# Kernel tuning notes

Measured on AMD Instinct MI355X. Metric: run time of the kernel, lower is better.

Reference implementation:

```python
import jax, jax.numpy as jnp
import numpy as np

B, C, H, W = 4, 128, 64, 64
HEADS, DH, MEM = 4, 32, 16
HID = HEADS * DH  # 128


def setup_inputs() -> dict:
    key = jax.random.key(0)
    k1, k2, k3, k4, k5 = jax.random.split(key, 5)
    return {
        "x": jax.random.normal(k1, (B, C, H, W), jnp.float32),
        "memory": jax.random.normal(k2, (1, C, 1, MEM), jnp.float32),
        "w_qkv": jax.random.normal(k3, (3 * HID, C), jnp.float32) * 0.05,  # conv1x1, bias=False
        "w_out": jax.random.normal(k4, (C, HID), jnp.float32) * 0.05,      # conv1x1 weight
        "b_out": jax.random.normal(k5, (C,), jnp.float32) * 0.01,          # conv1x1 bias
    }


def reference(x, memory, w_qkv, w_out, b_out):
    b, c, h, w = x.shape
    hw = h * w
    scale = DH ** -0.5

    # flatten spatial, append memory tokens along token axis
    x_flat = x.reshape(b, c, hw)                         # (b, c, hw)
    mem = jnp.broadcast_to(memory[:, :, 0, :], (b, c, MEM))
    x_ext = jnp.concatenate([x_flat, mem], axis=2)       # (b, c, n) n = hw + MEM

    # 1x1 conv QKV projection == channel matmul
    qkv = jnp.einsum('oc,bcn->bon', w_qkv, x_ext)        # (b, 3*HID, n)
    q, k, v = jnp.split(qkv, 3, axis=1)                  # each (b, HID, n)

    def to_heads(t):
        return t.reshape(b, HEADS, DH, -1)               # (b, h, d, n)

    q = to_heads(q) * scale
    k = to_heads(k)
    v = to_heads(v)

    sim = jnp.einsum('bhdi,bhdj->bhij', q, k)            # (b, h, n, n)
    attn = jax.nn.softmax(sim, axis=-1)                  # stable softmax (amax-sub inside)
    out = jnp.einsum('bhij,bhdj->bhid', attn, v)         # (b, h, n, d)

    out = out[:, :, :hw]                                 # drop memory-token queries
    out = out.transpose(0, 1, 3, 2).reshape(b, HID, h, w)  # b (h d) x y

    return jnp.einsum('oc,bchw->bohw', w_out, out) + b_out[None, :, None, None]
```

## Files before the change

### kernel.cpp

```cpp
#include <hip/hip_runtime.h>
#include <hip/hip_bf16.h>

constexpr int NQ   = 4096;
constexpr int NKV  = 4112;
constexpr int NP   = 4160;
constexpr int CDIM = 128;
constexpr float QSC = 0.17677669529663687f * 1.4426950408889634f;

typedef __attribute__((ext_vector_type(8)))  short bf16x8;
typedef __attribute__((ext_vector_type(4)))  short bf16x4;
typedef __attribute__((ext_vector_type(4)))  float f32x4;
typedef __attribute__((ext_vector_type(16))) float f32x16;

static __device__ __forceinline__ unsigned short bfbits(float f) {
  __hip_bfloat16 h = __float2bfloat16(f);
  return *reinterpret_cast<unsigned short*>(&h);
}
static __device__ __forceinline__ unsigned pk2(float a, float b) {
  return (unsigned)bfbits(a) | ((unsigned)bfbits(b) << 16);
}

__global__ __launch_bounds__(256) void k1_qkv(
    const float* __restrict__ x, const float* __restrict__ memry,
    const float* __restrict__ wqkv, const float* __restrict__ wout,
    __hip_bfloat16* __restrict__ Qt, __hip_bfloat16* __restrict__ Kt,
    __hip_bfloat16* __restrict__ Vt, __hip_bfloat16* __restrict__ Wb) {
  __shared__ __align__(16) __hip_bfloat16 xt[64][136];
  const int b  = blockIdx.y;
  const int nb = blockIdx.x * 64;
  const int t  = threadIdx.x;
  const int wv = t >> 6, ln = t & 63;

  if (blockIdx.x == 0 && b == 0) {
    for (int i = t; i < CDIM * CDIM; i += 256) Wb[i] = __float2bfloat16(wout[i]);
  }

  {
    const int n = nb + ln;
    #pragma unroll
    for (int i = 0; i < 16; ++i) {
      const int c = wv * 32 + 2 * i;
      float v0 = 0.f, v1 = 0.f;
      if (n < NQ)        { v0 = x[((size_t)b * CDIM + c) * NQ + n];
                           v1 = x[((size_t)b * CDIM + c + 1) * NQ + n]; }
      else if (n < NKV)  { v0 = memry[c * 16 + (n - NQ)];
                           v1 = memry[(c + 1) * 16 + (n - NQ)]; }
      *reinterpret_cast<unsigned*>(&xt[ln][c]) =
          (unsigned)bfbits(v0) | ((unsigned)bfbits(v1) << 16);
    }
  }
  __syncthreads();

  const int li = ln & 15, g = ln >> 4;
  bf16x8 xa[4][4];
  #pragma unroll
  for (int nt = 0; nt < 4; ++nt)
    #pragma unroll
    for (int k = 0; k < 4; ++k)
      xa[nt][k] = *reinterpret_cast<const bf16x8*>(&xt[nt * 16 + li][k * 32 + 8 * g]);

  #pragma unroll
  for (int oi = 0; oi < 6; ++oi) {
    const int ot = wv * 6 + oi;
    bf16x8 wf[4];
    #pragma unroll
    for (int k = 0; k < 4; ++k) {
      const float* wp = &wqkv[(size_t)(ot * 16 + li) * CDIM + k * 32 + 8 * g];
      const float4 f0 = *reinterpret_cast<const float4*>(wp);
      const float4 f1 = *reinterpret_cast<const float4*>(wp + 4);
      bf16x8 wc;
      wc[0] = (short)bfbits(f0.x); wc[1] = (short)bfbits(f0.y);
      wc[2] = (short)bfbits(f0.z); wc[3] = (short)bfbits(f0.w);
      wc[4] = (short)bfbits(f1.x); wc[5] = (short)bfbits(f1.y);
      wc[6] = (short)bfbits(f1.z); wc[7] = (short)bfbits(f1.w);
      wf[k] = wc;
    }
    #pragma unroll
    for (int nt = 0; nt < 4; ++nt) {
      f32x4 a; a[0] = a[1] = a[2] = a[3] = 0.f;
      if (ot < 16) {
        #pragma unroll
        for (int k = 0; k < 4; ++k)
          a = __builtin_amdgcn_mfma_f32_16x16x32_bf16(xa[nt][k], wf[k], a, 0, 0, 0);
        const int o = ot * 16 + li;
        const int h = (o >> 5) & 3, d = o & 31;
        if (ot < 8) {
          #pragma unroll
          for (int r = 0; r < 4; ++r) {
            const int n = nb + nt * 16 + 4 * g + r;
            Qt[((size_t)(b * 4 + h) * NP + n) * 32 + d] = __float2bfloat16(a[r] * QSC);
          }
        } else {
          #pragma unroll
          for (int r = 0; r < 4; ++r) {
            const int n = nb + nt * 16 + 4 * g + r;
            Kt[((size_t)(b * 4 + h) * NP + n) * 32 + d] = __float2bfloat16(a[r]);
          }
        }
      } else {
        #pragma unroll
        for (int k = 0; k < 4; ++k)
          a = __builtin_amdgcn_mfma_f32_16x16x32_bf16(wf[k], xa[nt][k], a, 0, 0, 0);
        #pragma unroll
        for (int r = 0; r < 4; ++r) {
          const int o = ot * 16 + 4 * g + r;
          const int h = (o >> 5) & 3, d = o & 31;
          const int n = nb + nt * 16 + li;
          Vt[((size_t)(b * 4 + h) * 32 + d) * NP + n] = __float2bfloat16(a[r]);
        }
      }
    }
  }
}


#if __has_builtin(__builtin_amdgcn_mfma_f32_32x32x8bf16_1k)
#define HAS_PV8 1
#else
#define HAS_PV8 0
#endif

__global__ __launch_bounds__(256, 2) void k2_attn(
    const __hip_bfloat16* __restrict__ Qt, const __hip_bfloat16* __restrict__ Kt,
    const __hip_bfloat16* __restrict__ Vt, __hip_bfloat16* __restrict__ att) {
  __shared__ __align__(16) unsigned char smem[16896];
  __hip_bfloat16* kbuf = (__hip_bfloat16*)smem;
  __hip_bfloat16* vbuf = (__hip_bfloat16*)(smem + 4096);
  float (*olds)[32][33] = (float(*)[32][33])smem;

  const int wg  = blockIdx.x;
  const int xcd = wg & 7;
  const int i   = wg >> 3;
  const int bh  = 2 * xcd + (i & 1);
  const int wv  = threadIdx.x >> 6, lane = threadIdx.x & 63;
  const int lq  = lane & 31, hi = lane >> 5;
  const int qb  = (i >> 1) * 128 + wv * 32;

  const bf16x8 qf0 = *reinterpret_cast<const bf16x8*>(
      Qt + ((size_t)bh * NP + qb + lq) * 32 + 8 * hi);
  const bf16x8 qf1 = *reinterpret_cast<const bf16x8*>(
      Qt + ((size_t)bh * NP + qb + lq) * 32 + 16 + 8 * hi);

  const __hip_bfloat16* Ksrc = Kt + ((size_t)bh * NP + (wv >> 1) * 32 + lq) * 32
                                  + (wv & 1) * 16 + 8 * hi;
  const __hip_bfloat16* Vsrc = Vt + ((size_t)bh * 32 + lq) * NP + wv * 16 + 8 * hi;
  __hip_bfloat16* kdst = kbuf + wv * 512 + lane * 8;
  __hip_bfloat16* vdst = vbuf + wv * 512 + lane * 8;

  f32x16 acc0, acc1, z;
  #pragma unroll
  for (int q = 0; q < 16; ++q) { acc0[q] = 0.f; acc1[q] = 0.f; z[q] = 0.f; }
  float l0 = 0.f, l1 = 0.f, l2 = 0.f, l3 = 0.f;

  bf16x8 kreg = *reinterpret_cast<const bf16x8*>(Ksrc);
  bf16x8 vreg = *reinterpret_cast<const bf16x8*>(Vsrc);

  for (int t = 0; t < 64; ++t) {
    *reinterpret_cast<bf16x8*>(kdst) = kreg;
    *reinterpret_cast<bf16x8*>(vdst) = vreg;
    __syncthreads();
    if (t < 63) {
      kreg = *reinterpret_cast<const bf16x8*>(Ksrc + (size_t)(t + 1) * 2048);
      vreg = *reinterpret_cast<const bf16x8*>(Vsrc + (t + 1) * 64);
    }
    #pragma unroll
    for (int st = 0; st < 2; ++st) {
      const bf16x8 kf0 = *reinterpret_cast<const bf16x8*>(kbuf + st * 1024 + lane * 8);
      const bf16x8 kf1 = *reinterpret_cast<const bf16x8*>(kbuf + st * 1024 + 512 + lane * 8);
      f32x16 s = __builtin_amdgcn_mfma_f32_32x32x16_bf16(kf0, qf0, z, 0, 0, 0);
      s = __builtin_amdgcn_mfma_f32_32x32x16_bf16(kf1, qf1, s, 0, 0, 0);
      float p[16];
      #pragma unroll
      for (int r = 0; r < 16; ++r) p[r] = __builtin_amdgcn_exp2f(s[r]);
      l0 += (p[0] + p[1]) + (p[2] + p[3]);
      l1 += (p[4] + p[5]) + (p[6] + p[7]);
      l2 += (p[8] + p[9]) + (p[10] + p[11]);
      l3 += (p[12] + p[13]) + (p[14] + p[15]);
#if HAS_PV8
      union UU { unsigned u[2]; bf16x4 v; };
      UU a0, a1, a2, a3;
      a0.u[0] = pk2(p[0], p[1]);   a0.u[1] = pk2(p[2], p[3]);
      a1.u[0] = pk2(p[4], p[5]);   a1.u[1] = pk2(p[6], p[7]);
      a2.u[0] = pk2(p[8], p[9]);   a2.u[1] = pk2(p[10], p[11]);
      a3.u[0] = pk2(p[12], p[13]); a3.u[1] = pk2(p[14], p[15]);
      const __hip_bfloat16* vb = vbuf + st * 1024 + lq * 8 + hi * 4;
      const bf16x4 vf0 = *reinterpret_cast<const bf16x4*>(vb);
      const bf16x4 vf1 = *reinterpret_cast<const bf16x4*>(vb + 256);
      const bf16x4 vf2 = *reinterpret_cast<const bf16x4*>(vb + 512);
      const bf16x4 vf3 = *reinterpret_cast<const bf16x4*>(vb + 768);
      acc0 = __builtin_amdgcn_mfma_f32_32x32x8bf16_1k(a0.v, vf0, acc0, 0, 0, 0);
      acc0 = __builtin_amdgcn_mfma_f32_32x32x8bf16_1k(a1.v, vf1, acc0, 0, 0, 0);
      acc1 = __builtin_amdgcn_mfma_f32_32x32x8bf16_1k(a2.v, vf2, acc1, 0, 0, 0);
      acc1 = __builtin_amdgcn_mfma_f32_32x32x8bf16_1k(a3.v, vf3, acc1, 0, 0, 0);
#else
      unsigned a0u0 = pk2(p[0], p[1]),   a0u1 = pk2(p[2], p[3]);
      unsigned a1u0 = pk2(p[4], p[5]),   a1u1 = pk2(p[6], p[7]);
      unsigned a2u0 = pk2(p[8], p[9]),   a2u1 = pk2(p[10], p[11]);
      unsigned a3u0 = pk2(p[12], p[13]), a3u1 = pk2(p[14], p[15]);
      union U8 { unsigned u[4]; bf16x8 v; };
      const bf16x8 vh0 = *reinterpret_cast<const bf16x8*>(vbuf + (2 * st) * 512 + lane * 8);
      const bf16x8 vh1 = *reinterpret_cast<const bf16x8*>(vbuf + (2 * st + 1) * 512 + lane * 8);
      {
        const unsigned s0 = __shfl_xor(hi ? a0u0 : a1u0, 32, 64);
        const unsigned s1 = __shfl_xor(hi ? a0u1 : a1u1, 32, 64);
        U8 f;
        f.u[0] = hi ? s0 : a0u0; f.u[1] = hi ? s1 : a0u1;
        f.u[2] = hi ? a1u0 : s0; f.u[3] = hi ? a1u1 : s1;
        acc0 = __builtin_amdgcn_mfma_f32_32x32x16_bf16(f.v, vh0, acc0, 0, 0, 0);
      }
      {
        const unsigned s0 = __shfl_xor(hi ? a2u0 : a3u0, 32, 64);
        const unsigned s1 = __shfl_xor(hi ? a2u1 : a3u1, 32, 64);
        U8 f;
        f.u[0] = hi ? s0 : a2u0; f.u[1] = hi ? s1 : a2u1;
        f.u[2] = hi ? a3u0 : s0; f.u[3] = hi ? a3u1 : s1;
        acc1 = __builtin_amdgcn_mfma_f32_32x32x16_bf16(f.v, vh1, acc1, 0, 0, 0);
      }
#endif
    }
    __syncthreads();
  }

  {
    const __hip_bfloat16* Kp   = Kt + (size_t)bh * NP * 32 + (size_t)lq * 32 + 8 * hi;
    const __hip_bfloat16* Vrow = Vt + ((size_t)bh * 32 + lq) * NP;
    const int kb = 4096;
    const bf16x8 kf0 = *reinterpret_cast<const bf16x8*>(Kp + (size_t)kb * 32);
    const bf16x8 kf1 = *reinterpret_cast<const bf16x8*>(Kp + (size_t)kb * 32 + 16);
    f32x16 s = __builtin_amdgcn_mfma_f32_32x32x16_bf16(kf0, qf0, z, 0, 0, 0);
    s = __builtin_amdgcn_mfma_f32_32x32x16_bf16(kf1, qf1, s, 0, 0, 0);
    float p[8];
    #pragma unroll
    for (int r = 0; r < 8; ++r) p[r] = __builtin_amdgcn_exp2f(s[r]);
    l0 += (p[0] + p[1]) + (p[2] + p[3]);
    l1 += (p[4] + p[5]) + (p[6] + p[7]);
#if HAS_PV8
    union UU { unsigned u[2]; bf16x4 v; };
    UU a0, a1;
    a0.u[0] = pk2(p[0], p[1]); a0.u[1] = pk2(p[2], p[3]);
    a1.u[0] = pk2(p[4], p[5]); a1.u[1] = pk2(p[6], p[7]);
    const bf16x4 vf0 = *reinterpret_cast<const bf16x4*>(Vrow + kb + 4 * hi);
    const bf16x4 vf1 = *reinterpret_cast<const bf16x4*>(Vrow + kb + 8 + 4 * hi);
    acc0 = __builtin_amdgcn_mfma_f32_32x32x8bf16_1k(a0.v, vf0, acc0, 0, 0, 0);
    acc0 = __builtin_amdgcn_mfma_f32_32x32x8bf16_1k(a1.v, vf1, acc0, 0, 0, 0);
#else
    unsigned a0u0 = pk2(p[0], p[1]), a0u1 = pk2(p[2], p[3]);
    unsigned a1u0 = pk2(p[4], p[5]), a1u1 = pk2(p[6], p[7]);
    union U8 { unsigned u[4]; bf16x8 v; };
    const unsigned s0 = __shfl_xor(hi ? a0u0 : a1u0, 32, 64);
    const unsigned s1 = __shfl_xor(hi ? a0u1 : a1u1, 32, 64);
    U8 f;
    f.u[0] = hi ? s0 : a0u0; f.u[1] = hi ? s1 : a0u1;
    f.u[2] = hi ? a1u0 : s0; f.u[3] = hi ? a1u1 : s1;
    const bf16x8 vf = *reinterpret_cast<const bf16x8*>(Vrow + kb + 8 * hi);
    acc0 = __builtin_amdgcn_mfma_f32_32x32x16_bf16(f.v, vf, acc0, 0, 0, 0);
#endif
  }

  float lsum = (l0 + l1) + (l2 + l3);
  lsum += __shfl_xor(lsum, 32, 64);
  const float inv = 1.f / lsum;

  __syncthreads();
  #pragma unroll
  for (int r = 0; r < 16; ++r)
    olds[wv][(r & 3) + 8 * (r >> 2) + 4 * hi][lq] = acc0[r] + acc1[r];
  __syncthreads();

  __hip_bfloat16* dst = att + ((size_t)bh * NQ + qb + lq) * 32 + hi * 16;
  unsigned wbuf[8];
  #pragma unroll
  for (int j = 0; j < 8; ++j)
    wbuf[j] = pk2(olds[wv][lq][hi * 16 + 2 * j] * inv,
                  olds[wv][lq][hi * 16 + 2 * j + 1] * inv);
  *reinterpret_cast<uint4*>(dst)     = make_uint4(wbuf[0], wbuf[1], wbuf[2], wbuf[3]);
  *reinterpret_cast<uint4*>(dst + 8) = make_uint4(wbuf[4], wbuf[5], wbuf[6], wbuf[7]);
}

__global__ __launch_bounds__(256) void k3_proj(
    const __hip_bfloat16* __restrict__ att, const __hip_bfloat16* __restrict__ Wb,
    const float* __restrict__ bout, float* __restrict__ out) {
  const int b = blockIdx.y, nb = blockIdx.x * 64;
  const int wv = threadIdx.x >> 6, lane = threadIdx.x & 63;
  const int li = lane & 15, g = lane >> 4;

  bf16x8 wf[2][4];
  float bo[2][4];
  #pragma unroll
  for (int tt = 0; tt < 2; ++tt) {
    const int ot = 2 * wv + tt;
    #pragma unroll
    for (int k = 0; k < 4; ++k)
      wf[tt][k] = *reinterpret_cast<const bf16x8*>(
          &Wb[(size_t)(ot * 16 + li) * CDIM + k * 32 + 8 * g]);
    #pragma unroll
    for (int r = 0; r < 4; ++r) bo[tt][r] = bout[ot * 16 + 4 * g + r];
  }
  #pragma unroll
  for (int nt = 0; nt < 4; ++nt) {
    bf16x8 bfr[4];
    #pragma unroll
    for (int k = 0; k < 4; ++k)
      bfr[k] = *reinterpret_cast<const bf16x8*>(
          &att[(((size_t)(b * 4 + k)) * NQ + nb + nt * 16 + li) * 32 + 8 * g]);
    #pragma unroll
    for (int tt = 0; tt < 2; ++tt) {
      f32x4 a; a[0] = a[1] = a[2] = a[3] = 0.f;
      #pragma unroll
      for (int k = 0; k < 4; ++k)
        a = __builtin_amdgcn_mfma_f32_16x16x32_bf16(wf[tt][k], bfr[k], a, 0, 0, 0);
      const int ot = 2 * wv + tt;
      #pragma unroll
      for (int r = 0; r < 4; ++r)
        out[((size_t)b * CDIM + ot * 16 + 4 * g + r) * NQ + nb + nt * 16 + li] =
            a[r] + bo[tt][r];
    }
  }
}

extern "C" void kernel_launch(void* const* d_in, const int* in_sizes, int n_in,
                              void* d_out, int out_size, void* d_ws, size_t ws_size,
                              hipStream_t stream) {
  const float* x    = (const float*)d_in[0];
  const float* memp = (const float*)d_in[1];
  const float* wqkv = (const float*)d_in[2];
  const float* wout = (const float*)d_in[3];
  const float* bout = (const float*)d_in[4];
  float* out = (float*)d_out;

  char* ws = (char*)d_ws;
  const size_t SZ  = (size_t)16 * NP * 32 * 2;
  const size_t ASZ = (size_t)16 * NQ * 32 * 2;
  __hip_bfloat16* Qt  = (__hip_bfloat16*)(ws);
  __hip_bfloat16* Kt  = (__hip_bfloat16*)(ws + SZ);
  __hip_bfloat16* Vt  = (__hip_bfloat16*)(ws + 2 * SZ);
  __hip_bfloat16* att = (__hip_bfloat16*)(ws + 3 * SZ);
  __hip_bfloat16* Wb  = (__hip_bfloat16*)(ws + 3 * SZ + ASZ);

  hipLaunchKernelGGL(k1_qkv, dim3(65, 4), dim3(256), 0, stream,
                     x, memp, wqkv, wout, Qt, Kt, Vt, Wb);
  hipLaunchKernelGGL(k2_attn, dim3(512), dim3(256), 0, stream, Qt, Kt, Vt, att);
  hipLaunchKernelGGL(k3_proj, dim3(64, 4), dim3(256), 0, stream, att, Wb, bout, out);
}
```

Baseline: 92.89 us.

## Split attention KV range across two workgroups with separate combine kernel

```diff
diff --git a/kernel.cpp b/kernel.cpp
--- a/kernel.cpp
+++ b/kernel.cpp
@@ -5,6 +5,7 @@
 constexpr int NKV  = 4112;
 constexpr int NP   = 4160;
 constexpr int CDIM = 128;
+constexpr int NSL  = 2;
 constexpr float QSC = 0.17677669529663687f * 1.4426950408889634f;
 
 typedef __attribute__((ext_vector_type(8)))  short bf16x8;
@@ -120,32 +121,31 @@
 #define HAS_PV8 0
 #endif
 
-__global__ __launch_bounds__(256, 2) void k2_attn(
+__global__ __launch_bounds__(256, 4) void k2_attn(
     const __hip_bfloat16* __restrict__ Qt, const __hip_bfloat16* __restrict__ Kt,
-    const __hip_bfloat16* __restrict__ Vt, __hip_bfloat16* __restrict__ att) {
-  __shared__ __align__(16) unsigned char smem[16896];
-  __hip_bfloat16* kbuf = (__hip_bfloat16*)smem;
-  __hip_bfloat16* vbuf = (__hip_bfloat16*)(smem + 4096);
-  float (*olds)[32][33] = (float(*)[32][33])smem;
+    const __hip_bfloat16* __restrict__ Vt, float* __restrict__ Pb,
+    float* __restrict__ Lb) {
+  __shared__ __align__(16) unsigned char smem[16384];
 
   const int wg  = blockIdx.x;
   const int xcd = wg & 7;
   const int i   = wg >> 3;
   const int bh  = 2 * xcd + (i & 1);
+  const int sl  = (i >> 1) & 1;
   const int wv  = threadIdx.x >> 6, lane = threadIdx.x & 63;
   const int lq  = lane & 31, hi = lane >> 5;
-  const int qb  = (i >> 1) * 128 + wv * 32;
+  const int qb  = (i >> 2) * 128 + wv * 32;
 
   const bf16x8 qf0 = *reinterpret_cast<const bf16x8*>(
       Qt + ((size_t)bh * NP + qb + lq) * 32 + 8 * hi);
   const bf16x8 qf1 = *reinterpret_cast<const bf16x8*>(
       Qt + ((size_t)bh * NP + qb + lq) * 32 + 16 + 8 * hi);
 
-  const __hip_bfloat16* Ksrc = Kt + ((size_t)bh * NP + (wv >> 1) * 32 + lq) * 32
+  const int kb0 = sl * 2048;
+  const __hip_bfloat16* Ksrc = Kt + ((size_t)bh * NP + kb0 + (wv >> 1) * 32 + lq) * 32
                                   + (wv & 1) * 16 + 8 * hi;
-  const __hip_bfloat16* Vsrc = Vt + ((size_t)bh * 32 + lq) * NP + wv * 16 + 8 * hi;
-  __hip_bfloat16* kdst = kbuf + wv * 512 + lane * 8;
-  __hip_bfloat16* vdst = vbuf + wv * 512 + lane * 8;
+  const __hip_bfloat16* Vsrc = Vt + ((size_t)bh * 32 + lq) * NP + kb0 + wv * 16 + 8 * hi;
+  const int dstoff = wv * 1024 + lane * 16;
 
   f32x16 acc0, acc1, z;
   #pragma unroll
@@ -154,35 +154,46 @@
 
   bf16x8 kreg = *reinterpret_cast<const bf16x8*>(Ksrc);
   bf16x8 vreg = *reinterpret_cast<const bf16x8*>(Vsrc);
-
-  for (int t = 0; t < 64; ++t) {
-    *reinterpret_cast<bf16x8*>(kdst) = kreg;
-    *reinterpret_cast<bf16x8*>(vdst) = vreg;
+  *reinterpret_cast<bf16x8*>(smem + dstoff)        = kreg;
+  *reinterpret_cast<bf16x8*>(smem + 4096 + dstoff) = vreg;
+  kreg = *reinterpret_cast<const bf16x8*>(Ksrc + 2048);
+  vreg = *reinterpret_cast<const bf16x8*>(Vsrc + 64);
+
+  for (int t = 0; t < 32; ++t) {
     __syncthreads();
-    if (t < 63) {
-      kreg = *reinterpret_cast<const bf16x8*>(Ksrc + (size_t)(t + 1) * 2048);
-      vreg = *reinterpret_cast<const bf16x8*>(Vsrc + (t + 1) * 64);
-    }
+    const int p = t & 1;
+    if (t < 31) {
+      unsigned char* nb = smem + (p ^ 1) * 8192;
+      *reinterpret_cast<bf16x8*>(nb + dstoff)        = kreg;
+      *reinterpret_cast<bf16x8*>(nb + 4096 + dstoff) = vreg;
+      if (t < 30) {
+        kreg = *reinterpret_cast<const bf16x8*>(Ksrc + (size_t)(t + 2) * 2048);
+        vreg = *reinterpret_cast<const bf16x8*>(Vsrc + (t + 2) * 64);
+      }
+    }
+    const __hip_bfloat16* kbuf = (const __hip_bfloat16*)(smem + p * 8192);
+    const __hip_bfloat16* vbuf = (const __hip_bfloat16*)(smem + p * 8192 + 4096);
+
     #pragma unroll
     for (int st = 0; st < 2; ++st) {
       const bf16x8 kf0 = *reinterpret_cast<const bf16x8*>(kbuf + st * 1024 + lane * 8);
       const bf16x8 kf1 = *reinterpret_cast<const bf16x8*>(kbuf + st * 1024 + 512 + lane * 8);
       f32x16 s = __builtin_amdgcn_mfma_f32_32x32x16_bf16(kf0, qf0, z, 0, 0, 0);
       s = __builtin_amdgcn_mfma_f32_32x32x16_bf16(kf1, qf1, s, 0, 0, 0);
-      float p[16];
+      float p_[16];
       #pragma unroll
-      for (int r = 0; r < 16; ++r) p[r] = __builtin_amdgcn_exp2f(s[r]);
-      l0 += (p[0] + p[1]) + (p[2] + p[3]);
-      l1 += (p[4] + p[5]) + (p[6] + p[7]);
-      l2 += (p[8] + p[9]) + (p[10] + p[11]);
-      l3 += (p[12] + p[13]) + (p[14] + p[15]);
+      for (int r = 0; r < 16; ++r) p_[r] = __builtin_amdgcn_exp2f(s[r]);
+      l0 += (p_[0] + p_[1]) + (p_[2] + p_[3]);
+      l1 += (p_[4] + p_[5]) + (p_[6] + p_[7]);
+      l2 += (p_[8] + p_[9]) + (p_[10] + p_[11]);
+      l3 += (p_[12] + p_[13]) + (p_[14] + p_[15]);
 #if HAS_PV8
       union UU { unsigned u[2]; bf16x4 v; };
       UU a0, a1, a2, a3;
-      a0.u[0] = pk2(p[0], p[1]);   a0.u[1] = pk2(p[2], p[3]);
-      a1.u[0] = pk2(p[4], p[5]);   a1.u[1] = pk2(p[6], p[7]);
-      a2.u[0] = pk2(p[8], p[9]);   a2.u[1] = pk2(p[10], p[11]);
-      a3.u[0] = pk2(p[12], p[13]); a3.u[1] = pk2(p[14], p[15]);
+      a0.u[0] = pk2(p_[0], p_[1]);   a0.u[1] = pk2(p_[2], p_[3]);
+      a1.u[0] = pk2(p_[4], p_[5]);   a1.u[1] = pk2(p_[6], p_[7]);
+      a2.u[0] = pk2(p_[8], p_[9]);   a2.u[1] = pk2(p_[10], p_[11]);
+      a3.u[0] = pk2(p_[12], p_[13]); a3.u[1] = pk2(p_[14], p_[15]);
       const __hip_bfloat16* vb = vbuf + st * 1024 + lq * 8 + hi * 4;
       const bf16x4 vf0 = *reinterpret_cast<const bf16x4*>(vb);
       const bf16x4 vf1 = *reinterpret_cast<const bf16x4*>(vb + 256);
@@ -193,10 +204,10 @@
       acc1 = __builtin_amdgcn_mfma_f32_32x32x8bf16_1k(a2.v, vf2, acc1, 0, 0, 0);
       acc1 = __builtin_amdgcn_mfma_f32_32x32x8bf16_1k(a3.v, vf3, acc1, 0, 0, 0);
 #else
-      unsigned a0u0 = pk2(p[0], p[1]),   a0u1 = pk2(p[2], p[3]);
-      unsigned a1u0 = pk2(p[4], p[5]),   a1u1 = pk2(p[6], p[7]);
-      unsigned a2u0 = pk2(p[8], p[9]),   a2u1 = pk2(p[10], p[11]);
-      unsigned a3u0 = pk2(p[12], p[13]), a3u1 = pk2(p[14], p[15]);
+      unsigned a0u0 = pk2(p_[0], p_[1]),   a0u1 = pk2(p_[2], p_[3]);
+      unsigned a1u0 = pk2(p_[4], p_[5]),   a1u1 = pk2(p_[6], p_[7]);
+      unsigned a2u0 = pk2(p_[8], p_[9]),   a2u1 = pk2(p_[10], p_[11]);
+      unsigned a3u0 = pk2(p_[12], p_[13]), a3u1 = pk2(p_[14], p_[15]);
       union U8 { unsigned u[4]; bf16x8 v; };
       const bf16x8 vh0 = *reinterpret_cast<const bf16x8*>(vbuf + (2 * st) * 512 + lane * 8);
       const bf16x8 vh1 = *reinterpret_cast<const bf16x8*>(vbuf + (2 * st + 1) * 512 + lane * 8);
@@ -218,10 +229,9 @@
       }
 #endif
     }
-    __syncthreads();
-  }
-
-  {
+  }
+
+  if (sl == NSL - 1) {
     const __hip_bfloat16* Kp   = Kt + (size_t)bh * NP * 32 + (size_t)lq * 32 + 8 * hi;
     const __hip_bfloat16* Vrow = Vt + ((size_t)bh * 32 + lq) * NP;
     const int kb = 4096;
@@ -229,23 +239,23 @@
     const bf16x8 kf1 = *reinterpret_cast<const bf16x8*>(Kp + (size_t)kb * 32 + 16);
     f32x16 s = __builtin_amdgcn_mfma_f32_32x32x16_bf16(kf0, qf0, z, 0, 0, 0);
     s = __builtin_amdgcn_mfma_f32_32x32x16_bf16(kf1, qf1, s, 0, 0, 0);
-    float p[8];
-    #pragma unroll
-    for (int r = 0; r < 8; ++r) p[r] = __builtin_amdgcn_exp2f(s[r]);
-    l0 += (p[0] + p[1]) + (p[2] + p[3]);
-    l1 += (p[4] + p[5]) + (p[6] + p[7]);
+    float p_[8];
+    #pragma unroll
+    for (int r = 0; r < 8; ++r) p_[r] = __builtin_amdgcn_exp2f(s[r]);
+    l0 += (p_[0] + p_[1]) + (p_[2] + p_[3]);
+    l1 += (p_[4] + p_[5]) + (p_[6] + p_[7]);
 #if HAS_PV8
     union UU { unsigned u[2]; bf16x4 v; };
     UU a0, a1;
-    a0.u[0] = pk2(p[0], p[1]); a0.u[1] = pk2(p[2], p[3]);
-    a1.u[0] = pk2(p[4], p[5]); a1.u[1] = pk2(p[6], p[7]);
+    a0.u[0] = pk2(p_[0], p_[1]); a0.u[1] = pk2(p_[2], p_[3]);
+    a1.u[0] = pk2(p_[4], p_[5]); a1.u[1] = pk2(p_[6], p_[7]);
     const bf16x4 vf0 = *reinterpret_cast<const bf16x4*>(Vrow + kb + 4 * hi);
     const bf16x4 vf1 = *reinterpret_cast<const bf16x4*>(Vrow + kb + 8 + 4 * hi);
     acc0 = __builtin_amdgcn_mfma_f32_32x32x8bf16_1k(a0.v, vf0, acc0, 0, 0, 0);
     acc0 = __builtin_amdgcn_mfma_f32_32x32x8bf16_1k(a1.v, vf1, acc0, 0, 0, 0);
 #else
-    unsigned a0u0 = pk2(p[0], p[1]), a0u1 = pk2(p[2], p[3]);
-    unsigned a1u0 = pk2(p[4], p[5]), a1u1 = pk2(p[6], p[7]);
+    unsigned a0u0 = pk2(p_[0], p_[1]), a0u1 = pk2(p_[2], p_[3]);
+    unsigned a1u0 = pk2(p_[4], p_[5]), a1u1 = pk2(p_[6], p_[7]);
     union U8 { unsigned u[4]; bf16x8 v; };
     const unsigned s0 = __shfl_xor(hi ? a0u0 : a1u0, 32, 64);
     const unsigned s1 = __shfl_xor(hi ? a0u1 : a1u1, 32, 64);
@@ -257,24 +267,55 @@
 #endif
   }
 
+  float* Pp = Pb + (((size_t)sl * 16 + bh) * NQ + qb) * 32;
+  #pragma unroll
+  for (int r = 0; r < 16; ++r) {
+    const int q = (r & 3) + 8 * (r >> 2) + 4 * hi;
+    Pp[(size_t)q * 32 + lq] = acc0[r] + acc1[r];
+  }
   float lsum = (l0 + l1) + (l2 + l3);
   lsum += __shfl_xor(lsum, 32, 64);
-  const float inv = 1.f / lsum;
-
-  __syncthreads();
-  #pragma unroll
-  for (int r = 0; r < 16; ++r)
-    olds[wv][(r & 3) + 8 * (r >> 2) + 4 * hi][lq] = acc0[r] + acc1[r];
-  __syncthreads();
-
-  __hip_bfloat16* dst = att + ((size_t)bh * NQ + qb + lq) * 32 + hi * 16;
-  unsigned wbuf[8];
-  #pragma unroll
-  for (int j = 0; j < 8; ++j)
-    wbuf[j] = pk2(olds[wv][lq][hi * 16 + 2 * j] * inv,
-                  olds[wv][lq][hi * 16 + 2 * j + 1] * inv);
-  *reinterpret_cast<uint4*>(dst)     = make_uint4(wbuf[0], wbuf[1], wbuf[2], wbuf[3]);
-  *reinterpret_cast<uint4*>(dst + 8) = make_uint4(wbuf[4], wbuf[5], wbuf[6], wbuf[7]);
+  if (hi == 0)
+    Lb[((size_t)sl * 16 + bh) * NQ + qb + lq] = lsum;
+}
+
+__global__ __launch_bounds__(256) void k2b_combine(
+    const float* __restrict__ Pb, const float* __restrict__ Lb,
+    __hip_bfloat16* __restrict__ att) {
+  const int idx = blockIdx.x * 256 + threadIdx.x;
+  const int bh = idx >> 12;
+  const int q  = idx & 4095;
+  constexpr size_t PS = (size_t)16 * NQ * 32;
+  constexpr size_t LS = (size_t)16 * NQ;
+  const float* p = Pb + ((size_t)bh * NQ + q) * 32;
+
+  float l = 0.f;
+  #pragma unroll
+  for (int s = 0; s < NSL; ++s) l += Lb[s * LS + (size_t)bh * NQ + q];
+  const float inv = 1.f / l;
+
+  float o[32];
+  #pragma unroll
+  for (int j = 0; j < 8; ++j) {
+    const float4 f = *reinterpret_cast<const float4*>(p + 4 * j);
+    o[4*j] = f.x; o[4*j+1] = f.y; o[4*j+2] = f.z; o[4*j+3] = f.w;
+  }
+  #pragma unroll
+  for (int s = 1; s < NSL; ++s)
+    #pragma unroll
+    for (int j = 0; j < 8; ++j) {
+      const float4 f = *reinterpret_cast<const float4*>(p + s * PS + 4 * j);
+      o[4*j] += f.x; o[4*j+1] += f.y; o[4*j+2] += f.z; o[4*j+3] += f.w;
+    }
+
+  unsigned wb[16];
+  #pragma unroll
+  for (int j = 0; j < 16; ++j) wb[j] = pk2(o[2*j] * inv, o[2*j+1] * inv);
+  __hip_bfloat16* dst = att + ((size_t)bh * NQ + q) * 32;
+  *reinterpret_cast<uint4*>(dst)      = make_uint4(wb[0],  wb[1],  wb[2],  wb[3]);
+  *reinterpret_cast<uint4*>(dst + 8)  = make_uint4(wb[4],  wb[5],  wb[6],  wb[7]);
+  *reinterpret_cast<uint4*>(dst + 16) = make_uint4(wb[8],  wb[9],  wb[10], wb[11]);
+  *reinterpret_cast<uint4*>(dst + 24) = make_uint4(wb[12], wb[13], wb[14], wb[15]);
 }
 
 __global__ __launch_bounds__(256) void k3_proj(
@@ -330,15 +371,21 @@
 
   char* ws = (char*)d_ws;
   const size_t SZ  = (size_t)16 * NP * 32 * 2;
+  const size_t PSZ = (size_t)NSL * 16 * NQ * 32 * 4;
+  const size_t LSZ = (size_t)NSL * 16 * NQ * 4;
   const size_t ASZ = (size_t)16 * NQ * 32 * 2;
   __hip_bfloat16* Qt  = (__hip_bfloat16*)(ws);
   __hip_bfloat16* Kt  = (__hip_bfloat16*)(ws + SZ);
   __hip_bfloat16* Vt  = (__hip_bfloat16*)(ws + 2 * SZ);
-  __hip_bfloat16* att = (__hip_bfloat16*)(ws + 3 * SZ);
-  __hip_bfloat16* Wb  = (__hip_bfloat16*)(ws + 3 * SZ + ASZ);
+  float*          Pbf = (float*)(ws + 3 * SZ);
+  float*          Lbf = (float*)(ws + 3 * SZ + PSZ);
+  __hip_bfloat16* att = (__hip_bfloat16*)(ws + 3 * SZ + PSZ + LSZ);
+  __hip_bfloat16* Wb  = (__hip_bfloat16*)(ws + 3 * SZ + PSZ + LSZ + ASZ);
 
   hipLaunchKernelGGL(k1_qkv, dim3(65, 4), dim3(256), 0, stream,
                      x, memp, wqkv, wout, Qt, Kt, Vt, Wb);
-  hipLaunchKernelGGL(k2_attn, dim3(512), dim3(256), 0, stream, Qt, Kt, Vt, att);
+  hipLaunchKernelGGL(k2_attn, dim3(1024), dim3(256), 0, stream,
+                     Qt, Kt, Vt, Pbf, Lbf);
+  hipLaunchKernelGGL(k2b_combine, dim3(256), dim3(256), 0, stream, Pbf, Lbf, att);
   hipLaunchKernelGGL(k3_proj, dim3(64, 4), dim3(256), 0, stream, att, Wb, bout, out);
 }
```

Result: slower. 98.04 us (+5.6%).
